# Kernel tuning notes

Hardware: AMD Instinct MI355X
Metric: run time of the kernel (lower is better)

Reference implementation:

```python
import jax, jax.numpy as jnp
import numpy as np
from jax import lax

DIM = 1024
HID = 2048          # dim * hidden_mult(2)
E = 8               # num_experts
K = 2               # top_k
B, T = 2, 512


def setup_inputs() -> dict:
    key = jax.random.key(0)
    ks = jax.random.split(key, 5)
    scale = 1.0 / np.sqrt(DIM)
    x = jax.random.normal(ks[0], (B, T, DIM), dtype=jnp.float32)
    router_w = jax.random.normal(ks[1], (E, DIM), dtype=jnp.float32) * scale   # Linear(dim, E) weight (out,in)
    w_gate = jax.random.normal(ks[2], (E, HID, DIM), dtype=jnp.float32) * scale
    w_up = jax.random.normal(ks[3], (E, HID, DIM), dtype=jnp.float32) * scale
    w_down = jax.random.normal(ks[4], (E, DIM, HID), dtype=jnp.float32) * (1.0 / np.sqrt(HID))
    return {"x": x, "router_w": router_w, "w_gate": w_gate, "w_up": w_up, "w_down": w_down}


def reference(x, router_w, w_gate, w_up, w_down):
    Bb, Tt, D = x.shape
    N = Bb * Tt
    xf = x.reshape(N, D)
    # router + top-k gating (weights renormalized over selected experts)
    logits = xf @ router_w.T                                   # (N, E)
    routing = jax.nn.softmax(logits, axis=-1)
    top_w, top_i = lax.top_k(routing, K)                       # (N, K)
    top_w = top_w / jnp.sum(top_w, axis=-1, keepdims=True)
    # combine weights: per-token weight for each expert (0 if not selected).
    # Multiplying by 0 reproduces the mask-gather-scatter loop exactly.
    combine = jnp.zeros((N, E), dtype=x.dtype)
    combine = combine.at[jnp.arange(N)[:, None], top_i].add(top_w)  # (N, E)
    # SwiGLU experts, batched over the (small, fixed) expert axis
    g = jnp.einsum('nd,ehd->neh', xf, w_gate)                  # (N, E, H)
    u = jnp.einsum('nd,ehd->neh', xf, w_up)
    h = jax.nn.silu(g) * u
    y = jnp.einsum('neh,edh->ned', h, w_down)                  # (N, E, D)
    out = jnp.einsum('ned,ne->nd', y, combine)
    return out.reshape(Bb, Tt, D)
```

## Files before the change

### kernel.cpp

```cpp
#include <hip/hip_runtime.h>
#include <hip/hip_bf16.h>
#include <math.h>

#define DIM 1024
#define HID 2048
#define NEXP 8
#define NTOK 1024
#define TOPK 2

typedef __attribute__((ext_vector_type(4))) float f32x4;
typedef __attribute__((ext_vector_type(8))) short bf16x8;
typedef __attribute__((ext_vector_type(4))) short bf16x4;

__device__ inline short bf1(float f) {
    union { __hip_bfloat16 b; short s; } u; u.b = __float2bfloat16(f); return u.s;
}
__device__ inline bf16x4 cvt4(f32x4 v) {
    bf16x4 r;
#pragma unroll
    for (int i = 0; i < 4; ++i) r[i] = bf1(v[i]);
    return r;
}
__device__ inline bf16x8 cat8(bf16x4 lo, bf16x4 hi) {
    bf16x8 r;
#pragma unroll
    for (int i = 0; i < 4; ++i) { r[i] = lo[i]; r[i + 4] = hi[i]; }
    return r;
}

__device__ __forceinline__ void gload16(const void* g, void* l) {
    __builtin_amdgcn_global_load_lds(
        (const __attribute__((address_space(1))) void*)g,
        (__attribute__((address_space(3))) void*)l,
        16, 0, 0);
}

__global__ __launch_bounds__(64) void router_kernel(
    const float* __restrict__ x, const float* __restrict__ rw,
    __hip_bfloat16* __restrict__ xb,
    int* __restrict__ counts, int* __restrict__ slot_list, float* __restrict__ w_list)
{
    int t = blockIdx.x;
    int lane = threadIdx.x;
    const float* xr = x + (size_t)t * DIM;
    f32x4 xv[4];
#pragma unroll
    for (int qq = 0; qq < 4; ++qq) xv[qq] = *(const f32x4*)(xr + qq * 256 + lane * 4);
#pragma unroll
    for (int qq = 0; qq < 4; ++qq)
        *(bf16x4*)(xb + (size_t)t * DIM + qq * 256 + lane * 4) = cvt4(xv[qq]);

    float acc[NEXP];
#pragma unroll
    for (int e = 0; e < NEXP; ++e) {
        const float* rwe = rw + e * DIM;
        f32x4 s4 = (f32x4)(0.f);
#pragma unroll
        for (int qq = 0; qq < 4; ++qq) {
            f32x4 wv = *(const f32x4*)(rwe + qq * 256 + lane * 4);
            s4 += xv[qq] * wv;
        }
        acc[e] = s4[0] + s4[1] + s4[2] + s4[3];
    }
#pragma unroll
    for (int off = 32; off > 0; off >>= 1) {
#pragma unroll
        for (int e = 0; e < NEXP; ++e) acc[e] += __shfl_down(acc[e], off, 64);
    }
    if (lane == 0) {
        int i1 = 0;
#pragma unroll
        for (int e = 1; e < NEXP; ++e) if (acc[e] > acc[i1]) i1 = e;
        int i2 = -1;
#pragma unroll
        for (int e = 0; e < NEXP; ++e) {
            if (e == i1) continue;
            if (i2 < 0 || acc[e] > acc[i2]) i2 = e;
        }
        float w1 = 1.f / (1.f + expf(acc[i2] - acc[i1]));
        float w2 = 1.f - w1;
        int p1 = atomicAdd(&counts[i1], 1);
        slot_list[i1 * NTOK + p1] = t * 2 + 0;
        w_list[i1 * NTOK + p1] = w1;
        int p2 = atomicAdd(&counts[i2], 1);
        slot_list[i2 * NTOK + p2] = t * 2 + 1;
        w_list[i2 * NTOK + p2] = w2;
    }
}

__global__ __launch_bounds__(256) void gateup_mfma(
    const __hip_bfloat16* __restrict__ xb, const float* __restrict__ wg,
    const float* __restrict__ wu, const int* __restrict__ counts,
    const int* __restrict__ slot_list, const float* __restrict__ w_list,
    const __hip_bfloat16* __restrict__ zrow, __hip_bfloat16* __restrict__ h_buf)
{
    __shared__ f32x4 ldsv[4][1024];

    int bid = blockIdx.x;
    int pl = bid & 7, sf = bid >> 3;
    int z = sf & 1;
    int s = ((sf >> 1) << 3) | pl;
    int e = s >> 6, strip = s & 63;
    int hb = strip * 32;

    int n_e = counts[e];
    const int* sl = slot_list + e * NTOK;
    const float* wl = w_list + e * NTOK;
    const float* WG = wg + (size_t)e * HID * DIM;
    const float* WU = wu + (size_t)e * HID * DIM;

    int tid = threadIdx.x, lane = tid & 63, wv = tid >> 6;
    int fr = lane & 15, fq = lane >> 4;
    int wm = wv >> 1, wn = wv & 1;

    int xr = lane >> 2, cX = lane & 3;
    int br = lane >> 3, cB = lane & 7;

    int rb0 = 2 * wv, rb1 = 2 * wv + 1;
    const float* bb0 = (rb0 < 4) ? (WG + (size_t)(hb + rb0 * 8 + br) * DIM)
                                 : (WU + (size_t)(hb + (rb0 - 4) * 8 + br) * DIM);
    const float* bb1 = (rb1 < 4) ? (WG + (size_t)(hb + rb1 * 8 + br) * DIM)
                                 : (WU + (size_t)(hb + (rb1 - 4) * 8 + br) * DIM);
    const char* pb0 = (const char*)bb0 + (cB ^ br) * 16;
    const char* pb1 = (const char*)bb1 + (cB ^ br) * 16;
    int sxg = ((cX - (xr >> 1)) & 3) * 16;

    char* b0 = (char*)&ldsv[0][0];

    for (int m0 = z * 128; m0 < n_e; m0 += 256) {
        int rows = n_e - m0; if (rows > 128) rows = 128;
        int r0 = 2 * wv * 16 + xr, r1 = r0 + 16;
        const char* px0 = (const char*)((r0 < rows) ? (xb + (size_t)(sl[m0 + r0] >> 1) * DIM) : zrow) + sxg;
        const char* px1 = (const char*)((r1 < rows) ? (xb + (size_t)(sl[m0 + r1] >> 1) * DIM) : zrow) + sxg;

        f32x4 accg[4], accu[4];
#pragma unroll
        for (int ms = 0; ms < 4; ++ms) { accg[ms] = (f32x4)(0.f); accu[ms] = (f32x4)(0.f); }

#pragma unroll
        for (int st = 0; st < 3; ++st) {
            char* dX = b0 + st * 16384 + (2 * wv) * 1024;
            gload16(px0 + st * 64, dX);
            gload16(px1 + st * 64, dX + 1024);
            char* dB = b0 + st * 16384 + 8192 + (2 * wv) * 1024;
            gload16(pb0 + st * 128, dB);
            gload16(pb1 + st * 128, dB + 1024);
        }

#pragma unroll 1
        for (int t = 0; t < 32; ++t) {
            if (t < 30)       asm volatile("s_waitcnt vmcnt(8)" ::: "memory");
            else if (t == 30) asm volatile("s_waitcnt vmcnt(4)" ::: "memory");
            else              asm volatile("s_waitcnt vmcnt(0)" ::: "memory");
            __builtin_amdgcn_s_barrier();

            const char* Xb = b0 + (t & 3) * 16384;
            const char* Bb = Xb + 8192;
            bf16x8 af[4];
#pragma unroll
            for (int ms = 0; ms < 4; ++ms) {
                int row = wm * 64 + ms * 16 + fr;
                int slot = (fq + (row >> 1)) & 3;
                af[ms] = *(const bf16x8*)(Xb + row * 64 + slot * 16);
            }
            int rg = wn * 16 + fr;
            f32x4 ga = *(const f32x4*)(Bb + rg * 128 + ((2 * fq) ^ (fr & 7)) * 16);
            f32x4 gb = *(const f32x4*)(Bb + rg * 128 + ((2 * fq + 1) ^ (fr & 7)) * 16);
            bf16x8 bgf = cat8(cvt4(ga), cvt4(gb));
            int ru = 32 + wn * 16 + fr;
            f32x4 ua = *(const f32x4*)(Bb + ru * 128 + ((2 * fq) ^ (fr & 7)) * 16);
            f32x4 ub = *(const f32x4*)(Bb + ru * 128 + ((2 * fq + 1) ^ (fr & 7)) * 16);
            bf16x8 buf_ = cat8(cvt4(ua), cvt4(ub));
#pragma unroll
            for (int ms = 0; ms < 4; ++ms) {
                accg[ms] = __builtin_amdgcn_mfma_f32_16x16x32_bf16(af[ms], bgf, accg[ms], 0, 0, 0);
                accu[ms] = __builtin_amdgcn_mfma_f32_16x16x32_bf16(af[ms], buf_, accu[ms], 0, 0, 0);
            }
            __builtin_amdgcn_s_barrier();

            if (t < 29) {
                int kt = t + 3, kb = kt & 3;
                char* dX = b0 + kb * 16384 + (2 * wv) * 1024;
                gload16(px0 + kt * 64, dX);
                gload16(px1 + kt * 64, dX + 1024);
                char* dB = b0 + kb * 16384 + 8192 + (2 * wv) * 1024;
                gload16(pb0 + kt * 128, dB);
                gload16(pb1 + kt * 128, dB + 1024);
            }
        }

#pragma unroll
        for (int ms = 0; ms < 4; ++ms) {
#pragma unroll
            for (int reg = 0; reg < 4; ++reg) {
                int r = wm * 64 + ms * 16 + fq * 4 + reg;
                if (r < rows) {
                    int slot = sl[m0 + r];
                    float w = wl[m0 + r];
                    float g = accg[ms][reg], u = accu[ms][reg];
                    float h = w * (g / (1.f + expf(-g))) * u;
                    h_buf[(size_t)slot * HID + hb + wn * 16 + fr] = __float2bfloat16(h);
                }
            }
        }
    }
}

__global__ __launch_bounds__(256) void down_mfma(
    const __hip_bfloat16* __restrict__ h_buf, const float* __restrict__ wd,
    const int* __restrict__ counts, const int* __restrict__ slot_list,
    const __hip_bfloat16* __restrict__ zrow, float* __restrict__ ybuf)
{
    __shared__ f32x4 ldsv[4][768];

    int bid = blockIdx.x;
    int pl = bid & 7, sf = bid >> 3;
    int z = sf & 1;
    int s = ((sf >> 1) << 3) | pl;
    int e = s >> 5, strip = s & 31;
    int db = strip * 32;

    int n_e = counts[e];
    const int* sl = slot_list + e * NTOK;
    const float* WD = wd + (size_t)e * DIM * HID;

    int tid = threadIdx.x, lane = tid & 63, wv = tid >> 6;
    int fr = lane & 15, fq = lane >> 4;
    int wm = wv >> 1, wn = wv & 1;

    int xr = lane >> 2, cX = lane & 3;
    int br = lane >> 3, cB = lane & 7;

    const char* pb = (const char*)(WD + (size_t)(db + wv * 8 + br) * HID) + (cB ^ br) * 16;
    int sxg = ((cX - (xr >> 1)) & 3) * 16;

    char* b0 = (char*)&ldsv[0][0];

    for (int m0 = z * 128; m0 < n_e; m0 += 256) {
        int rows = n_e - m0; if (rows > 128) rows = 128;
        int r0 = 2 * wv * 16 + xr, r1 = r0 + 16;
        const char* px0 = (const char*)((r0 < rows) ? (h_buf + (size_t)sl[m0 + r0] * HID) : zrow) + sxg;
        const char* px1 = (const char*)((r1 < rows) ? (h_buf + (size_t)sl[m0 + r1] * HID) : zrow) + sxg;

        f32x4 acc[4];
#pragma unroll
        for (int ms = 0; ms < 4; ++ms) acc[ms] = (f32x4)(0.f);

#pragma unroll
        for (int st = 0; st < 3; ++st) {
            char* dX = b0 + st * 12288 + (2 * wv) * 1024;
            gload16(px0 + st * 64, dX);
            gload16(px1 + st * 64, dX + 1024);
            gload16(pb + st * 128, b0 + st * 12288 + 8192 + wv * 1024);
        }

#pragma unroll 1
        for (int t = 0; t < 64; ++t) {
            if (t < 62)       asm volatile("s_waitcnt vmcnt(6)" ::: "memory");
            else if (t == 62) asm volatile("s_waitcnt vmcnt(3)" ::: "memory");
            else              asm volatile("s_waitcnt vmcnt(0)" ::: "memory");
            __builtin_amdgcn_s_barrier();

            const char* Hb = b0 + (t & 3) * 12288;
            const char* Bb = Hb + 8192;
            bf16x8 af[4];
#pragma unroll
            for (int ms = 0; ms < 4; ++ms) {
                int row = wm * 64 + ms * 16 + fr;
                int slot = (fq + (row >> 1)) & 3;
                af[ms] = *(const bf16x8*)(Hb + row * 64 + slot * 16);
            }
            int rb = wn * 16 + fr;
            f32x4 wa = *(const f32x4*)(Bb + rb * 128 + ((2 * fq) ^ (fr & 7)) * 16);
            f32x4 wb = *(const f32x4*)(Bb + rb * 128 + ((2 * fq + 1) ^ (fr & 7)) * 16);
            bf16x8 bw = cat8(cvt4(wa), cvt4(wb));
#pragma unroll
            for (int ms = 0; ms < 4; ++ms)
                acc[ms] = __builtin_amdgcn_mfma_f32_16x16x32_bf16(af[ms], bw, acc[ms], 0, 0, 0);

            __builtin_amdgcn_s_barrier();

            if (t < 61) {
                int kt = t + 3, kb = kt & 3;
                char* dX = b0 + kb * 12288 + (2 * wv) * 1024;
                gload16(px0 + kt * 64, dX);
                gload16(px1 + kt * 64, dX + 1024);
                gload16(pb + kt * 128, b0 + kb * 12288 + 8192 + wv * 1024);
            }
        }

#pragma unroll
        for (int ms = 0; ms < 4; ++ms) {
#pragma unroll
            for (int reg = 0; reg < 4; ++reg) {
                int r = wm * 64 + ms * 16 + fq * 4 + reg;
                if (r < rows) {
                    int slot = sl[m0 + r];
                    ybuf[(size_t)slot * DIM + db + wn * 16 + fr] = acc[ms][reg];
                }
            }
        }
    }
}

__global__ __launch_bounds__(256) void combine_kernel(const float* __restrict__ ybuf, float* __restrict__ out)
{
    int i = blockIdx.x * 256 + threadIdx.x;
    int t = i >> 8;
    int c = i & 255;
    const float4* ya = (const float4*)(ybuf + (size_t)(2 * t) * DIM) + c;
    const float4* yb = (const float4*)(ybuf + (size_t)(2 * t + 1) * DIM) + c;
    float4 a = *ya, b = *yb, r;
    r.x = a.x + b.x; r.y = a.y + b.y; r.z = a.z + b.z; r.w = a.w + b.w;
    ((float4*)(out + (size_t)t * DIM))[c] = r;
}

extern "C" void kernel_launch(void* const* d_in, const int* in_sizes, int n_in,
                              void* d_out, int out_size, void* d_ws, size_t ws_size,
                              hipStream_t stream) {
    const float* x  = (const float*)d_in[0];
    const float* rw = (const float*)d_in[1];
    const float* wg = (const float*)d_in[2];
    const float* wu = (const float*)d_in[3];
    const float* wd = (const float*)d_in[4];
    float* out = (float*)d_out;

    char* ws = (char*)d_ws;
    int* counts            = (int*)ws;
    int* slot_list         = (int*)(ws + 256);
    float* w_list          = (float*)(ws + 256 + NEXP * NTOK * 4);
    __hip_bfloat16* xb     = (__hip_bfloat16*)(ws + 256 + 2 * NEXP * NTOK * 4);
    __hip_bfloat16* h_buf  = (__hip_bfloat16*)((char*)xb + (size_t)NTOK * DIM * 2);
    float* ybuf            = (float*)((char*)h_buf + (size_t)NTOK * TOPK * HID * 2);
    __hip_bfloat16* zrow   = (__hip_bfloat16*)((char*)ybuf + (size_t)NTOK * TOPK * DIM * 4);

    hipMemsetAsync(counts, 0, NEXP * sizeof(int), stream);
    hipMemsetAsync(zrow, 0, HID * sizeof(__hip_bfloat16), stream);
    router_kernel<<<NTOK, 64, 0, stream>>>(x, rw, xb, counts, slot_list, w_list);
    gateup_mfma<<<1024, 256, 0, stream>>>(xb, wg, wu, counts, slot_list, w_list, zrow, h_buf);
    down_mfma<<<512, 256, 0, stream>>>(h_buf, wd, counts, slot_list, zrow, ybuf);
    combine_kernel<<<NTOK * DIM / 4 / 256, 256, 0, stream>>>(ybuf, out);
}
```

Measured before the change: 165.8 us.

## Stage converted weight strips in LDS once and stream token tiles

Both expert GEMM kernels now load their whole weight strip (16 output columns over the full K dimension) into LDS once, converting fp32 to bf16 as it goes. They then loop over 64-token tiles of the routed activations with a double-buffered pipeline. Previously weights were streamed from global memory per 128-token tile with a 4-stage buffer. The new scheme means each weight is read once per block, and blocks with empty experts exit early. The costs are smaller per-block tiles, much more LDS per block (lower occupancy), and serialised token tiles within a block.

```diff
diff --git a/kernel.cpp b/kernel.cpp
--- a/kernel.cpp
+++ b/kernel.cpp
@@ -94,16 +94,15 @@
     const int* __restrict__ slot_list, const float* __restrict__ w_list,
     const __hip_bfloat16* __restrict__ zrow, __hip_bfloat16* __restrict__ h_buf)
 {
-    __shared__ f32x4 ldsv[4][1024];
+    __shared__ short Bs[32 * 1024];
+    __shared__ short Xs[2][64 * 64];
 
     int bid = blockIdx.x;
-    int pl = bid & 7, sf = bid >> 3;
-    int z = sf & 1;
-    int s = ((sf >> 1) << 3) | pl;
-    int e = s >> 6, strip = s & 63;
-    int hb = strip * 32;
+    int e = bid >> 7;
+    int hb = (bid & 127) * 16;
 
     int n_e = counts[e];
+    if (n_e == 0) return;
     const int* sl = slot_list + e * NTOK;
     const float* wl = w_list + e * NTOK;
     const float* WG = wg + (size_t)e * HID * DIM;
@@ -111,96 +110,69 @@
 
     int tid = threadIdx.x, lane = tid & 63, wv = tid >> 6;
     int fr = lane & 15, fq = lane >> 4;
-    int wm = wv >> 1, wn = wv & 1;
-
-    int xr = lane >> 2, cX = lane & 3;
-    int br = lane >> 3, cB = lane & 7;
-
-    int rb0 = 2 * wv, rb1 = 2 * wv + 1;
-    const float* bb0 = (rb0 < 4) ? (WG + (size_t)(hb + rb0 * 8 + br) * DIM)
-                                 : (WU + (size_t)(hb + (rb0 - 4) * 8 + br) * DIM);
-    const float* bb1 = (rb1 < 4) ? (WG + (size_t)(hb + rb1 * 8 + br) * DIM)
-                                 : (WU + (size_t)(hb + (rb1 - 4) * 8 + br) * DIM);
-    const char* pb0 = (const char*)bb0 + (cB ^ br) * 16;
-    const char* pb1 = (const char*)bb1 + (cB ^ br) * 16;
-    int sxg = ((cX - (xr >> 1)) & 3) * 16;
-
-    char* b0 = (char*)&ldsv[0][0];
-
-    for (int m0 = z * 128; m0 < n_e; m0 += 256) {
-        int rows = n_e - m0; if (rows > 128) rows = 128;
-        int r0 = 2 * wv * 16 + xr, r1 = r0 + 16;
-        const char* px0 = (const char*)((r0 < rows) ? (xb + (size_t)(sl[m0 + r0] >> 1) * DIM) : zrow) + sxg;
-        const char* px1 = (const char*)((r1 < rows) ? (xb + (size_t)(sl[m0 + r1] >> 1) * DIM) : zrow) + sxg;
-
-        f32x4 accg[4], accu[4];
-#pragma unroll
-        for (int ms = 0; ms < 4; ++ms) { accg[ms] = (f32x4)(0.f); accu[ms] = (f32x4)(0.f); }
-
-#pragma unroll
-        for (int st = 0; st < 3; ++st) {
-            char* dX = b0 + st * 16384 + (2 * wv) * 1024;
-            gload16(px0 + st * 64, dX);
-            gload16(px1 + st * 64, dX + 1024);
-            char* dB = b0 + st * 16384 + 8192 + (2 * wv) * 1024;
-            gload16(pb0 + st * 128, dB);
-            gload16(pb1 + st * 128, dB + 1024);
-        }
-
-#pragma unroll 1
-        for (int t = 0; t < 32; ++t) {
-            if (t < 30)       asm volatile("s_waitcnt vmcnt(8)" ::: "memory");
-            else if (t == 30) asm volatile("s_waitcnt vmcnt(4)" ::: "memory");
-            else              asm volatile("s_waitcnt vmcnt(0)" ::: "memory");
-            __builtin_amdgcn_s_barrier();
-
-            const char* Xb = b0 + (t & 3) * 16384;
-            const char* Bb = Xb + 8192;
-            bf16x8 af[4];
-#pragma unroll
-            for (int ms = 0; ms < 4; ++ms) {
-                int row = wm * 64 + ms * 16 + fr;
-                int slot = (fq + (row >> 1)) & 3;
-                af[ms] = *(const bf16x8*)(Xb + row * 64 + slot * 16);
-            }
-            int rg = wn * 16 + fr;
-            f32x4 ga = *(const f32x4*)(Bb + rg * 128 + ((2 * fq) ^ (fr & 7)) * 16);
-            f32x4 gb = *(const f32x4*)(Bb + rg * 128 + ((2 * fq + 1) ^ (fr & 7)) * 16);
-            bf16x8 bgf = cat8(cvt4(ga), cvt4(gb));
-            int ru = 32 + wn * 16 + fr;
-            f32x4 ua = *(const f32x4*)(Bb + ru * 128 + ((2 * fq) ^ (fr & 7)) * 16);
-            f32x4 ub = *(const f32x4*)(Bb + ru * 128 + ((2 * fq + 1) ^ (fr & 7)) * 16);
-            bf16x8 buf_ = cat8(cvt4(ua), cvt4(ub));
-#pragma unroll
-            for (int ms = 0; ms < 4; ++ms) {
-                accg[ms] = __builtin_amdgcn_mfma_f32_16x16x32_bf16(af[ms], bgf, accg[ms], 0, 0, 0);
-                accu[ms] = __builtin_amdgcn_mfma_f32_16x16x32_bf16(af[ms], buf_, accu[ms], 0, 0, 0);
-            }
-            __builtin_amdgcn_s_barrier();
-
-            if (t < 29) {
-                int kt = t + 3, kb = kt & 3;
-                char* dX = b0 + kb * 16384 + (2 * wv) * 1024;
-                gload16(px0 + kt * 64, dX);
-                gload16(px1 + kt * 64, dX + 1024);
-                char* dB = b0 + kb * 16384 + 8192 + (2 * wv) * 1024;
-                gload16(pb0 + kt * 128, dB);
-                gload16(pb1 + kt * 128, dB + 1024);
-            }
-        }
-
-#pragma unroll
-        for (int ms = 0; ms < 4; ++ms) {
-#pragma unroll
-            for (int reg = 0; reg < 4; ++reg) {
-                int r = wm * 64 + ms * 16 + fq * 4 + reg;
-                if (r < rows) {
-                    int slot = sl[m0 + r];
-                    float w = wl[m0 + r];
-                    float g = accg[ms][reg], u = accu[ms][reg];
-                    float h = w * (g / (1.f + expf(-g))) * u;
-                    h_buf[(size_t)slot * HID + hb + wn * 16 + fr] = __float2bfloat16(h);
-                }
+
+#pragma unroll 4
+    for (int it = 0; it < 16; ++it) {
+        int dc = it * 256 + tid;
+        int r = dc >> 7;
+        int c = dc & 127;
+        const float* srow = (r < 16) ? (WG + (size_t)(hb + r) * DIM)
+                                     : (WU + (size_t)(hb + (r - 16)) * DIM);
+        f32x4 lo = *(const f32x4*)(srow + c * 8);
+        f32x4 hi = *(const f32x4*)(srow + c * 8 + 4);
+        *(bf16x8*)&Bs[r * 1024 + ((c ^ (r & 7)) * 8)] = cat8(cvt4(lo), cvt4(hi));
+    }
+    __syncthreads();
+
+    int rl = lane >> 3;
+    int soff = ((lane & 7) ^ rl) << 4;
+    char* dA = (char*)&Xs[0][0] + wv * 2048;
+
+    for (int m0 = 0; m0 < n_e; m0 += 64) {
+        int rows = n_e - m0; if (rows > 64) rows = 64;
+        int ra = wv * 16 + rl, rb = ra + 8;
+        const char* pa = (const char*)((ra < rows) ? (xb + (size_t)(sl[m0 + ra] >> 1) * DIM) : zrow) + soff;
+        const char* pb = (const char*)((rb < rows) ? (xb + (size_t)(sl[m0 + rb] >> 1) * DIM) : zrow) + soff;
+
+        f32x4 accg = (f32x4)(0.f), accu = (f32x4)(0.f);
+
+        gload16(pa, dA);              gload16(pb, dA + 1024);
+        gload16(pa + 128, dA + 8192); gload16(pb + 128, dA + 8192 + 1024);
+
+#pragma unroll
+        for (int t = 0; t < 16; ++t) {
+            if (t < 15) asm volatile("s_waitcnt vmcnt(2)" ::: "memory");
+            else        asm volatile("s_waitcnt vmcnt(0)" ::: "memory");
+            __builtin_amdgcn_s_barrier();
+            __builtin_amdgcn_sched_barrier(0);
+            const short* Xb = &Xs[t & 1][0];
+#pragma unroll
+            for (int kh = 0; kh < 2; ++kh) {
+                int sa = kh * 4 + fq;
+                bf16x8 a  = *(const bf16x8*)&Xb[(wv * 16 + fr) * 64 + ((sa ^ (fr & 7)) * 8)];
+                bf16x8 bg = *(const bf16x8*)&Bs[fr * 1024 + (((t * 8 + sa) ^ (fr & 7)) * 8)];
+                bf16x8 bu = *(const bf16x8*)&Bs[(16 + fr) * 1024 + (((t * 8 + sa) ^ (fr & 7)) * 8)];
+                accg = __builtin_amdgcn_mfma_f32_16x16x32_bf16(a, bg, accg, 0, 0, 0);
+                accu = __builtin_amdgcn_mfma_f32_16x16x32_bf16(a, bu, accu, 0, 0, 0);
+            }
+            __builtin_amdgcn_sched_barrier(0);
+            __builtin_amdgcn_s_barrier();
+            if (t < 14) {
+                char* dd = dA + (t & 1) * 8192;
+                gload16(pa + (t + 2) * 128, dd);
+                gload16(pb + (t + 2) * 128, dd + 1024);
+            }
+        }
+
+#pragma unroll
+        for (int reg = 0; reg < 4; ++reg) {
+            int r = wv * 16 + fq * 4 + reg;
+            if (r < rows) {
+                int slot = sl[m0 + r];
+                float w = wl[m0 + r];
+                float g = accg[reg], u = accu[reg];
+                float h = w * (g / (1.f + expf(-g))) * u;
+                h_buf[(size_t)slot * HID + hb + fr] = __float2bfloat16(h);
             }
         }
     }
@@ -211,93 +183,77 @@
     const int* __restrict__ counts, const int* __restrict__ slot_list,
     const __hip_bfloat16* __restrict__ zrow, float* __restrict__ ybuf)
 {
-    __shared__ f32x4 ldsv[4][768];
+    __shared__ short Bs[16 * 2048];
+    __shared__ short Hs[2][64 * 64];
 
     int bid = blockIdx.x;
-    int pl = bid & 7, sf = bid >> 3;
-    int z = sf & 1;
-    int s = ((sf >> 1) << 3) | pl;
-    int e = s >> 5, strip = s & 31;
-    int db = strip * 32;
+    int e = bid >> 6;
+    int db = (bid & 63) * 16;
 
     int n_e = counts[e];
+    if (n_e == 0) return;
     const int* sl = slot_list + e * NTOK;
     const float* WD = wd + (size_t)e * DIM * HID;
 
     int tid = threadIdx.x, lane = tid & 63, wv = tid >> 6;
     int fr = lane & 15, fq = lane >> 4;
-    int wm = wv >> 1, wn = wv & 1;
-
-    int xr = lane >> 2, cX = lane & 3;
-    int br = lane >> 3, cB = lane & 7;
-
-    const char* pb = (const char*)(WD + (size_t)(db + wv * 8 + br) * HID) + (cB ^ br) * 16;
-    int sxg = ((cX - (xr >> 1)) & 3) * 16;
-
-    char* b0 = (char*)&ldsv[0][0];
-
-    for (int m0 = z * 128; m0 < n_e; m0 += 256) {
-        int rows = n_e - m0; if (rows > 128) rows = 128;
-        int r0 = 2 * wv * 16 + xr, r1 = r0 + 16;
-        const char* px0 = (const char*)((r0 < rows) ? (h_buf + (size_t)sl[m0 + r0] * HID) : zrow) + sxg;
-        const char* px1 = (const char*)((r1 < rows) ? (h_buf + (size_t)sl[m0 + r1] * HID) : zrow) + sxg;
-
-        f32x4 acc[4];
-#pragma unroll
-        for (int ms = 0; ms < 4; ++ms) acc[ms] = (f32x4)(0.f);
-
-#pragma unroll
-        for (int st = 0; st < 3; ++st) {
-            char* dX = b0 + st * 12288 + (2 * wv) * 1024;
-            gload16(px0 + st * 64, dX);
-            gload16(px1 + st * 64, dX + 1024);
-            gload16(pb + st * 128, b0 + st * 12288 + 8192 + wv * 1024);
-        }
-
-#pragma unroll 1
-        for (int t = 0; t < 64; ++t) {
-            if (t < 62)       asm volatile("s_waitcnt vmcnt(6)" ::: "memory");
-            else if (t == 62) asm volatile("s_waitcnt vmcnt(3)" ::: "memory");
-            else              asm volatile("s_waitcnt vmcnt(0)" ::: "memory");
-            __builtin_amdgcn_s_barrier();
-
-            const char* Hb = b0 + (t & 3) * 12288;
-            const char* Bb = Hb + 8192;
-            bf16x8 af[4];
-#pragma unroll
-            for (int ms = 0; ms < 4; ++ms) {
-                int row = wm * 64 + ms * 16 + fr;
-                int slot = (fq + (row >> 1)) & 3;
-                af[ms] = *(const bf16x8*)(Hb + row * 64 + slot * 16);
-            }
-            int rb = wn * 16 + fr;
-            f32x4 wa = *(const f32x4*)(Bb + rb * 128 + ((2 * fq) ^ (fr & 7)) * 16);
-            f32x4 wb = *(const f32x4*)(Bb + rb * 128 + ((2 * fq + 1) ^ (fr & 7)) * 16);
-            bf16x8 bw = cat8(cvt4(wa), cvt4(wb));
-#pragma unroll
-            for (int ms = 0; ms < 4; ++ms)
-                acc[ms] = __builtin_amdgcn_mfma_f32_16x16x32_bf16(af[ms], bw, acc[ms], 0, 0, 0);
-
-            __builtin_amdgcn_s_barrier();
-
-            if (t < 61) {
-                int kt = t + 3, kb = kt & 3;
-                char* dX = b0 + kb * 12288 + (2 * wv) * 1024;
-                gload16(px0 + kt * 64, dX);
-                gload16(px1 + kt * 64, dX + 1024);
-                gload16(pb + kt * 128, b0 + kb * 12288 + 8192 + wv * 1024);
-            }
-        }
-
-#pragma unroll
-        for (int ms = 0; ms < 4; ++ms) {
-#pragma unroll
-            for (int reg = 0; reg < 4; ++reg) {
-                int r = wm * 64 + ms * 16 + fq * 4 + reg;
-                if (r < rows) {
-                    int slot = sl[m0 + r];
-                    ybuf[(size_t)slot * DIM + db + wn * 16 + fr] = acc[ms][reg];
-                }
+
+#pragma unroll 4
+    for (int it = 0; it < 16; ++it) {
+        int dc = it * 256 + tid;
+        int r = dc >> 8;
+        int c = dc & 255;
+        const float* srow = WD + (size_t)(db + r) * HID;
+        f32x4 lo = *(const f32x4*)(srow + c * 8);
+        f32x4 hi = *(const f32x4*)(srow + c * 8 + 4);
+        *(bf16x8*)&Bs[r * 2048 + ((c ^ (r & 7)) * 8)] = cat8(cvt4(lo), cvt4(hi));
+    }
+    __syncthreads();
+
+    int rl = lane >> 3;
+    int soff = ((lane & 7) ^ rl) << 4;
+    char* dA = (char*)&Hs[0][0] + wv * 2048;
+
+    for (int m0 = 0; m0 < n_e; m0 += 64) {
+        int rows = n_e - m0; if (rows > 64) rows = 64;
+        int ra = wv * 16 + rl, rb = ra + 8;
+        const char* pa = (const char*)((ra < rows) ? (h_buf + (size_t)sl[m0 + ra] * HID) : zrow) + soff;
+        const char* pb = (const char*)((rb < rows) ? (h_buf + (size_t)sl[m0 + rb] * HID) : zrow) + soff;
+
+        f32x4 acc = (f32x4)(0.f);
+
+        gload16(pa, dA);              gload16(pb, dA + 1024);
+        gload16(pa + 128, dA + 8192); gload16(pb + 128, dA + 8192 + 1024);
+
+#pragma unroll
+        for (int t = 0; t < 32; ++t) {
+            if (t < 31) asm volatile("s_waitcnt vmcnt(2)" ::: "memory");
+            else        asm volatile("s_waitcnt vmcnt(0)" ::: "memory");
+            __builtin_amdgcn_s_barrier();
+            __builtin_amdgcn_sched_barrier(0);
+            const short* Hb = &Hs[t & 1][0];
+#pragma unroll
+            for (int kh = 0; kh < 2; ++kh) {
+                int sa = kh * 4 + fq;
+                bf16x8 a = *(const bf16x8*)&Hb[(wv * 16 + fr) * 64 + ((sa ^ (fr & 7)) * 8)];
+                bf16x8 b = *(const bf16x8*)&Bs[fr * 2048 + (((t * 8 + sa) ^ (fr & 7)) * 8)];
+                acc = __builtin_amdgcn_mfma_f32_16x16x32_bf16(a, b, acc, 0, 0, 0);
+            }
+            __builtin_amdgcn_sched_barrier(0);
+            __builtin_amdgcn_s_barrier();
+            if (t < 30) {
+                char* dd = dA + (t & 1) * 8192;
+                gload16(pa + (t + 2) * 128, dd);
+                gload16(pb + (t + 2) * 128, dd + 1024);
+            }
+        }
+
+#pragma unroll
+        for (int reg = 0; reg < 4; ++reg) {
+            int r = wv * 16 + fq * 4 + reg;
+            if (r < rows) {
+                int slot = sl[m0 + r];
+                ybuf[(size_t)slot * DIM + db + fr] = acc[reg];
             }
         }
     }
```

Measured after the change: 223.8 us. 35.0% more time.
